# Kernel optimization log

Measured on AMD Instinct MI355X. Metric: run time of the kernel, lower is better.

## Reference

```python
import jax, jax.numpy as jnp
import numpy as np


def _conv1x1(w, x):
    # w: [out, in], x: [B, in, H, W] -> [B, out, H, W]
    return jnp.einsum('oc,bchw->bohw', w, x)


def _maxpool2(x):
    # 2x2 max pool, stride 2. x: [B, C, H, W] -> [B, C, H//2, W//2]
    B, C, H, W = x.shape
    return x.reshape(B, C, H // 2, 2, W // 2, 2).max(axis=(3, 5))


def setup_inputs() -> dict:
    key = jax.random.key(0)
    ks = jax.random.split(key, 5)
    B, C, H, W = 8, 256, 64, 64
    div = 8
    x = jax.random.normal(ks[0], (B, C, H, W), dtype=jnp.float32)
    wq = jax.random.normal(ks[1], (C // div, C), dtype=jnp.float32) * (C ** -0.5)
    wk = jax.random.normal(ks[2], (C // div, C), dtype=jnp.float32) * (C ** -0.5)
    wv = jax.random.normal(ks[3], (C // 2, C), dtype=jnp.float32) * (C ** -0.5)
    wo = jax.random.normal(ks[4], (C, C // 2), dtype=jnp.float32) * ((C // 2) ** -0.5)
    gamma = jnp.float32(0.5)  # nonzero so attention branch contributes
    return {"x": x, "wq": wq, "wk": wk, "wv": wv, "wo": wo, "gamma": gamma}


def reference(x, wq, wk, wv, wo, gamma):
    B, C, H, W = x.shape
    HW = H * W
    # query: [B, HW, Cq]
    q = _conv1x1(wq, x).reshape(B, -1, HW).transpose(0, 2, 1)
    # key: maxpool -> [B, Cq, HW//4]
    k = _maxpool2(_conv1x1(wk, x)).reshape(B, -1, HW // 4)
    # value: maxpool -> [B, C//2, HW//4]
    v = _maxpool2(_conv1x1(wv, x)).reshape(B, -1, HW // 4)
    scores = jnp.einsum('bnc,bcm->bnm', q, k)          # [B, HW, HW//4]
    attn = jax.nn.softmax(scores, axis=2)
    ctx = jnp.einsum('bcm,bnm->bcn', v, attn)          # [B, C//2, HW]
    ctx = ctx.reshape(B, C // 2, H, W)
    out = gamma * _conv1x1(wo, ctx) + x
    return out
```

## Files before the change

### kernel.cpp

```cpp
#include <hip/hip_runtime.h>
#include <hip/hip_bf16.h>

#define BB  8
#define CC  256
#define HW  4096
#define CQ  32
#define CV  128
#define MP  1024

#define XT_OFF  0
#define Y_OFF   4194304
#define KT_OFF  (Y_OFF + 3145728)
#define VP_OFF  (KT_OFF + 131072)
#define CT_OFF  (VP_OFF + 524288)

typedef __attribute__((ext_vector_type(8))) short bf16x8;
typedef __attribute__((ext_vector_type(4))) short short4v;
typedef __attribute__((ext_vector_type(4))) float f32x4;

__device__ __forceinline__ short f2b(float f) {
    unsigned u = __float_as_uint(f);
    u += 0x7fffu + ((u >> 16) & 1u);
    return (short)(u >> 16);
}
__device__ __forceinline__ float b2f(short s) {
    return __uint_as_float(((unsigned)(unsigned short)s) << 16);
}

__global__ __launch_bounds__(256) void k_xt(
    const float* __restrict__ x, short* __restrict__ xt)
{
    __shared__ float t[64][65];
    const int bid = blockIdx.x;
    const int nt = bid & 63;
    const int ct = (bid >> 6) & 3;
    const int b  = bid >> 8;
    const int c0 = ct * 64, n0 = nt * 64;
    const int tid = threadIdx.x;

    const int col = tid & 63, wrow = (tid >> 6) * 16;
    #pragma unroll
    for (int i = 0; i < 16; ++i) {
        int r = wrow + i;
        t[r][col] = x[((long)(b * CC + c0 + r)) * HW + n0 + col];
    }
    __syncthreads();

    const int n = tid >> 2, cb = (tid & 3) * 16;
    short buf[16];
    #pragma unroll
    for (int j = 0; j < 16; ++j) buf[j] = f2b(t[cb + j][n]);
    short* dst = &xt[((long)(b * HW + n0 + n)) * CC + c0 + cb];
    *(int4*)dst = *(int4*)&buf[0];
    *(int4*)(dst + 8) = *(int4*)&buf[8];
}

__global__ __launch_bounds__(256) void k_qkv(
    const float* __restrict__ wq, const float* __restrict__ wk,
    const float* __restrict__ wv, const short* __restrict__ xt,
    short* __restrict__ y)
{
    __shared__ short w_lds[96 * 264];
    __shared__ short x_lds[256 * 40];
    const int bid = blockIdx.x;
    const int oc = bid & 1;
    const int nt = (bid >> 1) & 15;
    const int b  = bid >> 5;
    const int o0 = oc * 96, n0 = nt * 256;
    const int tid = threadIdx.x;
    const int lane = tid & 63;
    const int wvid = tid >> 6;
    const int l15 = lane & 15, g = lane >> 4;

    for (int it = 0; it < 24; ++it) {
        int idx = tid + it * 256;
        int ol = idx >> 6, cq = (idx & 63) * 4;
        int o = o0 + ol;
        const float* src = (o < 32) ? &wq[o * 256 + cq]
                         : (o < 64) ? &wk[(o - 32) * 256 + cq]
                                    : &wv[(o - 64) * 256 + cq];
        float4 w = *(const float4*)src;
        short4v p = { f2b(w.x), f2b(w.y), f2b(w.z), f2b(w.w) };
        *(short4v*)&w_lds[ol * 264 + cq] = p;
    }

    f32x4 acc[4][6];
    #pragma unroll
    for (int nf = 0; nf < 4; ++nf)
        #pragma unroll
        for (int of = 0; of < 6; ++of) acc[nf][of] = (f32x4){0.f, 0.f, 0.f, 0.f};

    for (int ks = 0; ks < 8; ++ks) {
        __syncthreads();
        {
            const short* src = &xt[((long)(b * HW + n0 + tid)) * CC + ks * 32];
            int4 v0 = *(const int4*)src;
            int4 v1 = *(const int4*)(src + 8);
            int4 v2 = *(const int4*)(src + 16);
            int4 v3 = *(const int4*)(src + 24);
            short* dst = &x_lds[tid * 40];
            *(int4*)dst = v0; *(int4*)(dst + 8) = v1;
            *(int4*)(dst + 16) = v2; *(int4*)(dst + 24) = v3;
        }
        __syncthreads();

        bf16x8 a[4], bf[6];
        #pragma unroll
        for (int nf = 0; nf < 4; ++nf)
            a[nf] = *(const bf16x8*)&x_lds[(wvid * 64 + nf * 16 + l15) * 40 + 8 * g];
        #pragma unroll
        for (int of = 0; of < 6; ++of)
            bf[of] = *(const bf16x8*)&w_lds[(of * 16 + l15) * 264 + ks * 32 + 8 * g];
        #pragma unroll
        for (int nf = 0; nf < 4; ++nf)
            #pragma unroll
            for (int of = 0; of < 6; ++of)
                acc[nf][of] = __builtin_amdgcn_mfma_f32_16x16x32_bf16(a[nf], bf[of], acc[nf][of], 0, 0, 0);
    }

    #pragma unroll
    for (int nf = 0; nf < 4; ++nf) {
        #pragma unroll
        for (int of = 0; of < 6; ++of) {
            int o = o0 + of * 16 + l15;
            long nb = (long)(b * HW + n0 + wvid * 64 + nf * 16 + 4 * g);
            #pragma unroll
            for (int r = 0; r < 4; ++r)
                y[(nb + r) * 192 + o] = f2b(acc[nf][of][r]);
        }
    }
}

__global__ __launch_bounds__(256) void k_pool(
    const short* __restrict__ y, short* __restrict__ kT, short* __restrict__ vp)
{
    __shared__ short t[64 * 136];
    const int bid = blockIdx.x;
    const int mt = bid & 15;
    const int b  = bid >> 4;
    const int m0 = mt * 64;
    const int tid = threadIdx.x;

    {
        int ml = tid >> 2, ci = (tid & 3) * 8;
        int pp = m0 + ml;
        int ph = pp >> 5, pw = pp & 31;
        const short* src = &y[((long)(b * HW) + ph * 128 + pw * 2) * 192 + 32 + ci];
        int4 s0 = *(const int4*)src;
        int4 s1 = *(const int4*)(src + 192);
        int4 s2 = *(const int4*)(src + 12288);
        int4 s3 = *(const int4*)(src + 12480);
        const short *a = (const short*)&s0, *bb = (const short*)&s1,
                    *c = (const short*)&s2, *d = (const short*)&s3;
        short o8[8];
        #pragma unroll
        for (int j = 0; j < 8; ++j)
            o8[j] = f2b(fmaxf(fmaxf(b2f(a[j]), b2f(bb[j])), fmaxf(b2f(c[j]), b2f(d[j]))));
        *(int4*)&kT[((long)(b * MP + pp)) * CQ + ci] = *(int4*)o8;
    }
    #pragma unroll
    for (int jj = 0; jj < 4; ++jj) {
        int idx = tid + jj * 256;
        int ml = idx >> 4, ci = (idx & 15) * 8;
        int pp = m0 + ml;
        int ph = pp >> 5, pw = pp & 31;
        const short* src = &y[((long)(b * HW) + ph * 128 + pw * 2) * 192 + 64 + ci];
        int4 s0 = *(const int4*)src;
        int4 s1 = *(const int4*)(src + 192);
        int4 s2 = *(const int4*)(src + 12288);
        int4 s3 = *(const int4*)(src + 12480);
        const short *a = (const short*)&s0, *bb = (const short*)&s1,
                    *c = (const short*)&s2, *d = (const short*)&s3;
        short o8[8];
        #pragma unroll
        for (int j = 0; j < 8; ++j)
            o8[j] = f2b(fmaxf(fmaxf(b2f(a[j]), b2f(bb[j])), fmaxf(b2f(c[j]), b2f(d[j]))));
        *(int4*)&t[ml * 136 + ci] = *(int4*)o8;
    }
    __syncthreads();
    {
        int c = tid & 127, mc = (tid >> 7) * 32;
        short buf[32];
        #pragma unroll
        for (int mm = 0; mm < 32; ++mm) buf[mm] = t[(mc + mm) * 136 + c];
        short* dst = &vp[((long)(b * CV + c)) * MP + m0 + mc];
        *(int4*)dst = *(int4*)&buf[0];
        *(int4*)(dst + 8)  = *(int4*)&buf[8];
        *(int4*)(dst + 16) = *(int4*)&buf[16];
        *(int4*)(dst + 24) = *(int4*)&buf[24];
    }
}

__global__ __launch_bounds__(128) void k_attn(
    const short* __restrict__ y,
    const short* __restrict__ kT,
    const short* __restrict__ vp,
    short* __restrict__ ctx)
{
    __shared__ short p_lds[2][2][16][40];
    const int tid  = threadIdx.x;
    const int lane = tid & 63;
    const int wid  = tid >> 6;
    const int b    = blockIdx.x >> 6;
    const int q0   = (blockIdx.x & 63) * 64 + wid * 32;
    const int l15  = lane & 15;
    const int g    = lane >> 4;

    bf16x8 qf[2];
    const short* yq = y + (long)b * HW * 192;
    #pragma unroll
    for (int si = 0; si < 2; ++si)
        qf[si] = *(const bf16x8*)&yq[(long)(q0 + si * 16 + l15) * 192 + 8 * g];

    float m_run[2] = {-INFINITY, -INFINITY};
    float l_run[2] = {0.f, 0.f};
    f32x4 acc[2][8];
    #pragma unroll
    for (int si = 0; si < 2; ++si)
        #pragma unroll
        for (int ct = 0; ct < 8; ++ct)
            acc[si][ct] = (f32x4){0.f, 0.f, 0.f, 0.f};

    const short* kTb = kT + (long)b * MP * CQ;
    const short* vpb = vp + (long)b * CV * MP;

    for (int mt = 0; mt < 32; ++mt) {
        const int m0 = mt * 32;
        bf16x8 ka0 = *(const bf16x8*)&kTb[(m0 + l15) * CQ + 8 * g];
        bf16x8 ka1 = *(const bf16x8*)&kTb[(m0 + 16 + l15) * CQ + 8 * g];
        bf16x8 va[8];
        #pragma unroll
        for (int ct = 0; ct < 8; ++ct)
            va[ct] = *(const bf16x8*)&vpb[(ct * 16 + l15) * MP + m0 + 8 * g];

        #pragma unroll
        for (int si = 0; si < 2; ++si) {
            f32x4 s0 = (f32x4){0.f, 0.f, 0.f, 0.f};
            f32x4 s1 = (f32x4){0.f, 0.f, 0.f, 0.f};
            s0 = __builtin_amdgcn_mfma_f32_16x16x32_bf16(ka0, qf[si], s0, 0, 0, 0);
            s1 = __builtin_amdgcn_mfma_f32_16x16x32_bf16(ka1, qf[si], s1, 0, 0, 0);
            float tmax = fmaxf(fmaxf(fmaxf(s0[0], s0[1]), fmaxf(s0[2], s0[3])),
                               fmaxf(fmaxf(s1[0], s1[1]), fmaxf(s1[2], s1[3])));
            tmax = fmaxf(tmax, __shfl_xor(tmax, 16, 64));
            tmax = fmaxf(tmax, __shfl_xor(tmax, 32, 64));
            float mr = m_run[si];
            if (!__all(tmax <= mr + 8.0f)) {
                float nm = fmaxf(mr, tmax);
                float alpha = __expf(mr - nm);
                l_run[si] *= alpha;
                #pragma unroll
                for (int r = 0; r < 4; ++r) {
                    float ar = __shfl(alpha, 4 * g + r, 64);
                    #pragma unroll
                    for (int ct = 0; ct < 8; ++ct) acc[si][ct][r] *= ar;
                }
                m_run[si] = nm;
                mr = nm;
            }
            float p[8];
            #pragma unroll
            for (int r = 0; r < 4; ++r) { p[r] = __expf(s0[r] - mr); p[4 + r] = __expf(s1[r] - mr); }
            float ts = ((p[0] + p[1]) + (p[2] + p[3])) + ((p[4] + p[5]) + (p[6] + p[7]));
            ts += __shfl_xor(ts, 16, 64);
            ts += __shfl_xor(ts, 32, 64);
            l_run[si] += ts;
            short4v w0 = { f2b(p[0]), f2b(p[1]), f2b(p[2]), f2b(p[3]) };
            short4v w1 = { f2b(p[4]), f2b(p[5]), f2b(p[6]), f2b(p[7]) };
            *(short4v*)&p_lds[wid][si][l15][4 * g]      = w0;
            *(short4v*)&p_lds[wid][si][l15][16 + 4 * g] = w1;
        }
        #pragma unroll
        for (int si = 0; si < 2; ++si) {
            bf16x8 pf = *(const bf16x8*)&p_lds[wid][si][l15][8 * g];
            #pragma unroll
            for (int ct = 0; ct < 8; ++ct)
                acc[si][ct] = __builtin_amdgcn_mfma_f32_16x16x32_bf16(pf, va[ct], acc[si][ct], 0, 0, 0);
        }
    }

    #pragma unroll
    for (int si = 0; si < 2; ++si) {
        float inv = 1.f / l_run[si];
        #pragma unroll
        for (int r = 0; r < 4; ++r) {
            float invr = __shfl(inv, 4 * g + r, 64);
            long q = q0 + si * 16 + 4 * g + r;
            short* cb = &ctx[((long)b * HW + q) * CV];
            #pragma unroll
            for (int ct = 0; ct < 8; ++ct)
                cb[ct * 16 + l15] = f2b(acc[si][ct][r] * invr);
        }
    }
}

__global__ __launch_bounds__(256) void k_out(
    const short* __restrict__ ctx, const float* __restrict__ wo,
    const float* __restrict__ x, const float* __restrict__ gamma,
    float* __restrict__ out)
{
    __shared__ short c_lds[256 * 136];
    __shared__ short w_lds[128 * 136];
    const int bid = blockIdx.x;
    const int oc = bid & 1;
    const int nt = (bid >> 1) & 15;
    const int b  = bid >> 5;
    const int o0 = oc * 128, n0 = nt * 256;
    const int tid = threadIdx.x;
    const int lane = tid & 63;
    const int l15 = lane & 15, g = lane >> 4;

    {
        const short* src = &ctx[((long)(b * HW + n0 + tid)) * CV];
        short* dst = &c_lds[tid * 136];
        #pragma unroll
        for (int j = 0; j < 16; ++j)
            *(int4*)(dst + 8 * j) = *(const int4*)(src + 8 * j);
    }
    for (int it = 0; it < 16; ++it) {
        int idx = tid + it * 256;
        int ol = idx >> 5, cq = (idx & 31) * 4;
        float4 w = *(const float4*)&wo[(o0 + ol) * CV + cq];
        short4v p = { f2b(w.x), f2b(w.y), f2b(w.z), f2b(w.w) };
        *(short4v*)&w_lds[ol * 136 + cq] = p;
    }
    __syncthreads();

    const int wvid = tid >> 6;
    const int ow = (wvid & 1) * 64, nw = (wvid >> 1) * 128;
    f32x4 acc[4][8];
    #pragma unroll
    for (int of = 0; of < 4; ++of)
        #pragma unroll
        for (int nf = 0; nf < 8; ++nf) acc[of][nf] = (f32x4){0.f, 0.f, 0.f, 0.f};

    #pragma unroll
    for (int ks = 0; ks < 4; ++ks) {
        bf16x8 af[4], bf[8];
        #pragma unroll
        for (int of = 0; of < 4; ++of)
            af[of] = *(const bf16x8*)&w_lds[(ow + of * 16 + l15) * 136 + ks * 32 + 8 * g];
        #pragma unroll
        for (int nf = 0; nf < 8; ++nf)
            bf[nf] = *(const bf16x8*)&c_lds[(nw + nf * 16 + l15) * 136 + ks * 32 + 8 * g];
        #pragma unroll
        for (int of = 0; of < 4; ++of)
            #pragma unroll
            for (int nf = 0; nf < 8; ++nf)
                acc[of][nf] = __builtin_amdgcn_mfma_f32_16x16x32_bf16(af[of], bf[nf], acc[of][nf], 0, 0, 0);
    }

    const float gma = gamma[0];
    #pragma unroll
    for (int of = 0; of < 4; ++of) {
        #pragma unroll
        for (int r = 0; r < 4; ++r) {
            int o = o0 + ow + of * 16 + 4 * g + r;
            #pragma unroll
            for (int nf = 0; nf < 8; ++nf) {
                int n = n0 + nw + nf * 16 + l15;
                long idx = (long)(b * CC + o) * HW + n;
                out[idx] = gma * acc[of][nf][r] + x[idx];
            }
        }
    }
}

extern "C" void kernel_launch(void* const* d_in, const int* in_sizes, int n_in,
                              void* d_out, int out_size, void* d_ws, size_t ws_size,
                              hipStream_t stream) {
    const float* x     = (const float*)d_in[0];
    const float* wq    = (const float*)d_in[1];
    const float* wk    = (const float*)d_in[2];
    const float* wv    = (const float*)d_in[3];
    const float* wo    = (const float*)d_in[4];
    const float* gamma = (const float*)d_in[5];
    float* out = (float*)d_out;
    float* ws  = (float*)d_ws;

    short* xt  = (short*)(ws + XT_OFF);
    short* y   = (short*)(ws + Y_OFF);
    short* kT  = (short*)(ws + KT_OFF);
    short* vp  = (short*)(ws + VP_OFF);
    short* ctx = (short*)(ws + CT_OFF);

    k_xt  <<<dim3(2048), dim3(256), 0, stream>>>(x, xt);
    k_qkv <<<dim3(256),  dim3(256), 0, stream>>>(wq, wk, wv, xt, y);
    k_pool<<<dim3(128),  dim3(256), 0, stream>>>(y, kT, vp);
    k_attn<<<dim3(512),  dim3(128), 0, stream>>>(y, kT, vp, ctx);
    k_out <<<dim3(256),  dim3(256), 0, stream>>>(ctx, wo, x, gamma, out);
}
```

Measured before the change: 98.32 us.

## Split attention key dimension across waves and merge softmax partials in LDS

The attention kernel now gives each 256-thread block 32 queries and splits the 1024 keys across four waves (split-K flash attention). Each wave keeps its own running max and sum, then the partials are rescaled and reduced through shared memory before a vectorized bf16 store of ctx. This doubles the block count and shortens each wave's serial loop to raise parallelism and occupancy on the GPU. In exchange it adds LDS traffic, extra barriers and a combine step, and each query tile is loaded by all four waves.

```diff
diff --git a/kernel.cpp b/kernel.cpp
--- a/kernel.cpp
+++ b/kernel.cpp
@@ -191,18 +191,22 @@
     }
 }
 
-__global__ __launch_bounds__(128) void k_attn(
+__global__ __launch_bounds__(256, 4) void k_attn(
     const short* __restrict__ y,
     const short* __restrict__ kT,
     const short* __restrict__ vp,
     short* __restrict__ ctx)
 {
-    __shared__ short p_lds[2][2][16][40];
+    __shared__ union {
+        short p[4][2][16][40];
+        float facc[4][16][132];
+    } sm;
+    __shared__ float sml[4][2][16][2];
     const int tid  = threadIdx.x;
     const int lane = tid & 63;
     const int wid  = tid >> 6;
-    const int b    = blockIdx.x >> 6;
-    const int q0   = (blockIdx.x & 63) * 64 + wid * 32;
+    const int b    = blockIdx.x >> 7;
+    const int q0   = (blockIdx.x & 127) * 32;
     const int l15  = lane & 15;
     const int g    = lane >> 4;
 
@@ -224,8 +228,8 @@
     const short* kTb = kT + (long)b * MP * CQ;
     const short* vpb = vp + (long)b * CV * MP;
 
-    for (int mt = 0; mt < 32; ++mt) {
-        const int m0 = mt * 32;
+    for (int t = 0; t < 8; ++t) {
+        const int m0 = wid * 256 + t * 32;
         bf16x8 ka0 = *(const bf16x8*)&kTb[(m0 + l15) * CQ + 8 * g];
         bf16x8 ka1 = *(const bf16x8*)&kTb[(m0 + 16 + l15) * CQ + 8 * g];
         bf16x8 va[8];
@@ -266,30 +270,61 @@
             l_run[si] += ts;
             short4v w0 = { f2b(p[0]), f2b(p[1]), f2b(p[2]), f2b(p[3]) };
             short4v w1 = { f2b(p[4]), f2b(p[5]), f2b(p[6]), f2b(p[7]) };
-            *(short4v*)&p_lds[wid][si][l15][4 * g]      = w0;
-            *(short4v*)&p_lds[wid][si][l15][16 + 4 * g] = w1;
+            *(short4v*)&sm.p[wid][si][l15][4 * g]      = w0;
+            *(short4v*)&sm.p[wid][si][l15][16 + 4 * g] = w1;
         }
         #pragma unroll
         for (int si = 0; si < 2; ++si) {
-            bf16x8 pf = *(const bf16x8*)&p_lds[wid][si][l15][8 * g];
+            bf16x8 pf = *(const bf16x8*)&sm.p[wid][si][l15][8 * g];
             #pragma unroll
             for (int ct = 0; ct < 8; ++ct)
                 acc[si][ct] = __builtin_amdgcn_mfma_f32_16x16x32_bf16(pf, va[ct], acc[si][ct], 0, 0, 0);
         }
     }
 
-    #pragma unroll
+    if (lane < 16) {
+        sml[wid][0][lane][0] = m_run[0]; sml[wid][0][lane][1] = l_run[0];
+        sml[wid][1][lane][0] = m_run[1]; sml[wid][1][lane][1] = l_run[1];
+    }
+    __syncthreads();
+
     for (int si = 0; si < 2; ++si) {
-        float inv = 1.f / l_run[si];
-        #pragma unroll
-        for (int r = 0; r < 4; ++r) {
-            float invr = __shfl(inv, 4 * g + r, 64);
-            long q = q0 + si * 16 + 4 * g + r;
-            short* cb = &ctx[((long)b * HW + q) * CV];
-            #pragma unroll
-            for (int ct = 0; ct < 8; ++ct)
-                cb[ct * 16 + l15] = f2b(acc[si][ct][r] * invr);
-        }
+        float M = sml[0][si][l15][0];
+        M = fmaxf(M, sml[1][si][l15][0]);
+        M = fmaxf(M, sml[2][si][l15][0]);
+        M = fmaxf(M, sml[3][si][l15][0]);
+        float mysc = __expf(m_run[si] - M);
+        float sc[4];
+        #pragma unroll
+        for (int r = 0; r < 4; ++r) sc[r] = __shfl(mysc, 4 * g + r, 64);
+        #pragma unroll
+        for (int ct = 0; ct < 8; ++ct)
+            #pragma unroll
+            for (int r = 0; r < 4; ++r)
+                sm.facc[wid][4 * g + r][ct * 16 + l15] = acc[si][ct][r] * sc[r];
+        __syncthreads();
+
+        {
+            int q = tid >> 4, c0 = (tid & 15) * 8;
+            float Mq = sml[0][si][q][0];
+            Mq = fmaxf(Mq, sml[1][si][q][0]);
+            Mq = fmaxf(Mq, sml[2][si][q][0]);
+            Mq = fmaxf(Mq, sml[3][si][q][0]);
+            float Lq = sml[0][si][q][1] * __expf(sml[0][si][q][0] - Mq)
+                     + sml[1][si][q][1] * __expf(sml[1][si][q][0] - Mq)
+                     + sml[2][si][q][1] * __expf(sml[2][si][q][0] - Mq)
+                     + sml[3][si][q][1] * __expf(sml[3][si][q][0] - Mq);
+            float inv = 1.f / Lq;
+            short o8[8];
+            #pragma unroll
+            for (int j = 0; j < 8; ++j) {
+                float s = sm.facc[0][q][c0 + j] + sm.facc[1][q][c0 + j]
+                        + sm.facc[2][q][c0 + j] + sm.facc[3][q][c0 + j];
+                o8[j] = f2b(s * inv);
+            }
+            *(int4*)&ctx[((long)(b * HW + q0 + si * 16 + q)) * CV + c0] = *(int4*)o8;
+        }
+        __syncthreads();
     }
 }
 
@@ -386,6 +421,6 @@
     k_xt  <<<dim3(2048), dim3(256), 0, stream>>>(x, xt);
     k_qkv <<<dim3(256),  dim3(256), 0, stream>>>(wq, wk, wv, xt, y);
     k_pool<<<dim3(128),  dim3(256), 0, stream>>>(y, kT, vp);
-    k_attn<<<dim3(512),  dim3(128), 0, stream>>>(y, kT, vp, ctx);
+    k_attn<<<dim3(1024), dim3(256), 0, stream>>>(y, kT, vp, ctx);
     k_out <<<dim3(256),  dim3(256), 0, stream>>>(ctx, wo, x, gamma, out);
 }
```

Result: slower. 111.7 us (+13.6%).
